# Kernel tuning notes

Hardware: AMD Instinct MI355X
Metric: run time of the kernel (lower is better)

The kernel has to match this reference:

```python
import jax, jax.numpy as jnp
import numpy as np

B, T, D = 4, 1024, 1024
H, DH = 8, 128           # heads, dim_head = dim // heads
E, FF = 8, 2048          # num_experts, expert hidden_dim
LN_EPS = 1e-5


def setup_inputs() -> dict:
    key = jax.random.key(0)
    ks = jax.random.split(key, 20)
    s = 0.02
    inp = {
        'v': jax.random.normal(ks[0], (B, T, D), jnp.float32),
        'k': jax.random.normal(ks[1], (B, T, D), jnp.float32),
        'q': jax.random.normal(ks[2], (B, T, D), jnp.float32),
        'noise': jax.random.normal(ks[3], (B * T, E), jnp.float32),
        # LayerNorm params (norm_v, norm_k, norm_q, norm_moe, moe output norm)
        'g_v': jnp.ones((D,)), 'b_v': jnp.zeros((D,)),
        'g_k': jnp.ones((D,)), 'b_k': jnp.zeros((D,)),
        'g_q': jnp.ones((D,)), 'b_q': jnp.zeros((D,)),
        'g_moe': jnp.ones((D,)), 'b_moe': jnp.zeros((D,)),
        'g_out': jnp.ones((D,)), 'b_out': jnp.zeros((D,)),
        # LinearAttention projections (q/k/v have no bias, out_proj has bias)
        'Wq': jax.random.normal(ks[4], (D, H * DH), jnp.float32) * s,
        'Wk': jax.random.normal(ks[5], (D, H * DH), jnp.float32) * s,
        'Wv': jax.random.normal(ks[6], (D, H * DH), jnp.float32) * s,
        'Wo': jax.random.normal(ks[7], (H * DH, D), jnp.float32) * s,
        'bo': jnp.zeros((D,)),
        # Router
        'Wr': jax.random.normal(ks[8], (D, E), jnp.float32) * s,
        'br': jnp.zeros((E,)),
        # Experts (stacked): dim -> FF -> dim
        'W1': jax.random.normal(ks[9], (E, D, FF), jnp.float32) * s,
        'b1': jnp.zeros((E, FF)),
        'W2': jax.random.normal(ks[10], (E, FF, D), jnp.float32) * s,
        'b2': jnp.zeros((E, D)),
        'top_k': 2,
    }
    return inp


def _ln(x, g, b):
    mu = x.mean(-1, keepdims=True)
    x0 = x - mu
    var = (x0 * x0).mean(-1, keepdims=True)
    return x0 * jax.lax.rsqrt(var + LN_EPS) * g + b


def reference(v, k, q, noise, g_v, b_v, g_k, b_k, g_q, b_q, g_moe, b_moe,
              g_out, b_out, Wq, Wk, Wv, Wo, bo, Wr, br, W1, b1, W2, b2, top_k):
    # --- LinearAttention over pre-normed v,k,q ---
    qh = jnp.einsum('btd,de->bte', _ln(q, g_q, b_q), Wq).reshape(B, T, H, DH)
    kh = jnp.einsum('btd,de->bte', _ln(k, g_k, b_k), Wk).reshape(B, T, H, DH)
    vh = jnp.einsum('btd,de->bte', _ln(v, g_v, b_v), Wv).reshape(B, T, H, DH)
    qf = jax.nn.elu(qh) + 1.0
    kf = jax.nn.elu(kh) + 1.0
    kv = jnp.einsum('bthd,bthe->bhde', kf, vh)          # [B,H,DH,DH]
    out = jnp.einsum('bthd,bhde->bthe', qf, kv)         # [B,T,H,DH]
    k_sum = kf.sum(axis=1) + 1e-6                       # [B,H,DH]
    denom = jnp.einsum('bthd,bhd->bth', qf, k_sum)[..., None]
    out = out / denom
    attn_out = jnp.einsum('bte,ed->btd', out.reshape(B, T, H * DH), Wo) + bo

    q_res = q + attn_out

    # --- MoEBlock: noisy top-k routing + expert MLPs + residual + LayerNorm ---
    x = _ln(q_res, g_moe, b_moe)
    xf = x.reshape(B * T, D)
    logits = xf @ Wr + br + noise * 0.1                 # noisy gating (randn/10)
    scores = jax.nn.softmax(logits, axis=-1)
    topk_s, topk_i = jax.lax.top_k(scores, top_k)       # [N,K]
    combine = (jax.nn.one_hot(topk_i, E, dtype=scores.dtype) * topk_s[..., None]).sum(1)  # [N,E]
    h = jax.nn.gelu(jnp.einsum('nd,edh->enh', xf, W1) + b1[:, None, :], approximate=False)
    eo = jnp.einsum('enh,ehd->end', h, W2) + b2[:, None, :]
    moe = jnp.einsum('end,ne->nd', eo, combine)         # weighted combine == masked dispatch
    moe_out = _ln(moe.reshape(B, T, D) + x, g_out, b_out)

    return q_res + moe_out
```

## Files before the change

kernel.cpp:

```cpp
#include <hip/hip_runtime.h>
#include <math.h>

typedef __attribute__((ext_vector_type(8))) short short8;
typedef __attribute__((ext_vector_type(4))) float f32x4;

#define LN_EPS 1e-5f

__device__ __forceinline__ float bf2f(unsigned short u) {
  unsigned int x = ((unsigned int)u) << 16;
  float f;
  __builtin_memcpy(&f, &x, 4);
  return f;
}
__device__ __forceinline__ unsigned short f2bf(float f) {
  unsigned int x;
  __builtin_memcpy(&x, &f, 4);
  x += 0x7fffu + ((x >> 16) & 1u);
  return (unsigned short)(x >> 16);
}

__device__ __forceinline__ void gload16(const void* g, void* l) {
  __builtin_amdgcn_global_load_lds(
      (__attribute__((address_space(1))) void*)(void*)g,
      (__attribute__((address_space(3))) void*)l, 16, 0, 0);
}

__device__ __forceinline__ void xcd_swizzle(int& bx, int& by) {
  const int nx = gridDim.x;
  const int nwg = nx * gridDim.y;
  const int orig = blockIdx.y * nx + blockIdx.x;
  const int cpx = nwg >> 3;
  const int lid = (orig & 7) * cpx + (orig >> 3);
  bx = lid % nx;
  by = lid / nx;
}

__device__ __forceinline__ void blockReduce2(float& a, float& b, float* s8) {
#pragma unroll
  for (int off = 32; off > 0; off >>= 1) {
    a += __shfl_down(a, off);
    b += __shfl_down(b, off);
  }
  const int w = threadIdx.x >> 6;
  if ((threadIdx.x & 63) == 0) { s8[w] = a; s8[4 + w] = b; }
  __syncthreads();
  a = s8[0] + s8[1] + s8[2] + s8[3];
  b = s8[4] + s8[5] + s8[6] + s8[7];
}

__global__ __launch_bounds__(256) void ln3_kernel(
    const float* __restrict__ q, const float* __restrict__ k, const float* __restrict__ v,
    const float* __restrict__ gq, const float* __restrict__ bq,
    const float* __restrict__ gk, const float* __restrict__ bk,
    const float* __restrict__ gv, const float* __restrict__ bv,
    unsigned short* __restrict__ oq, unsigned short* __restrict__ ok,
    unsigned short* __restrict__ ov) {
  __shared__ float s8[8];
  const int row = blockIdx.x, which = blockIdx.y;
  const float* x = which == 0 ? q : which == 1 ? k : v;
  const float* g = which == 0 ? gq : which == 1 ? gk : gv;
  const float* b = which == 0 ? bq : which == 1 ? bk : bv;
  unsigned short* o = which == 0 ? oq : which == 1 ? ok : ov;
  const float4 xv = ((const float4*)(x + (size_t)row * 1024))[threadIdx.x];
  float s = xv.x + xv.y + xv.z + xv.w;
  float s2 = xv.x * xv.x + xv.y * xv.y + xv.z * xv.z + xv.w * xv.w;
  blockReduce2(s, s2, s8);
  const float mu = s * (1.f / 1024.f);
  const float rs = rsqrtf(s2 * (1.f / 1024.f) - mu * mu + LN_EPS);
  const int c = threadIdx.x * 4;
  const float y[4] = {xv.x, xv.y, xv.z, xv.w};
#pragma unroll
  for (int j = 0; j < 4; ++j)
    o[(size_t)row * 1024 + c + j] = f2bf((y[j] - mu) * rs * g[c + j] + b[c + j]);
}

__global__ __launch_bounds__(256) void ln_moe_router_kernel(
    const float* __restrict__ qres, const float* __restrict__ g, const float* __restrict__ b,
    const float* __restrict__ Wr, const float* __restrict__ br,
    const float* __restrict__ noise,
    float* __restrict__ xf, unsigned short* __restrict__ xb,
    int* __restrict__ pick, float* __restrict__ pw) {
  __shared__ float s8[8];
  __shared__ float sacc[32];
  const int row = blockIdx.x;
  const float4 xv = ((const float4*)(qres + (size_t)row * 1024))[threadIdx.x];
  float s = xv.x + xv.y + xv.z + xv.w;
  float s2 = xv.x * xv.x + xv.y * xv.y + xv.z * xv.z + xv.w * xv.w;
  blockReduce2(s, s2, s8);
  const float mu = s * (1.f / 1024.f);
  const float rs = rsqrtf(s2 * (1.f / 1024.f) - mu * mu + LN_EPS);
  const int c = threadIdx.x * 4;
  const float yin[4] = {xv.x, xv.y, xv.z, xv.w};
  float y[4];
#pragma unroll
  for (int j = 0; j < 4; ++j) {
    y[j] = (yin[j] - mu) * rs * g[c + j] + b[c + j];
    xf[(size_t)row * 1024 + c + j] = y[j];
    xb[(size_t)row * 1024 + c + j] = f2bf(y[j]);
  }
  float acc[8] = {};
  const float4* wrv = (const float4*)(Wr + (size_t)c * 8);
#pragma unroll
  for (int j = 0; j < 4; ++j) {
    const float4 w0 = wrv[j * 2], w1 = wrv[j * 2 + 1];
    acc[0] += y[j] * w0.x; acc[1] += y[j] * w0.y;
    acc[2] += y[j] * w0.z; acc[3] += y[j] * w0.w;
    acc[4] += y[j] * w1.x; acc[5] += y[j] * w1.y;
    acc[6] += y[j] * w1.z; acc[7] += y[j] * w1.w;
  }
#pragma unroll
  for (int off = 32; off > 0; off >>= 1)
#pragma unroll
    for (int e = 0; e < 8; ++e) acc[e] += __shfl_down(acc[e], off);
  const int w = threadIdx.x >> 6;
  if ((threadIdx.x & 63) == 0)
#pragma unroll
    for (int e = 0; e < 8; ++e) sacc[w * 8 + e] = acc[e];
  __syncthreads();
  if (threadIdx.x == 0) {
    float lg[8], mx = -1e30f;
#pragma unroll
    for (int e = 0; e < 8; ++e) {
      lg[e] = sacc[e] + sacc[8 + e] + sacc[16 + e] + sacc[24 + e] + br[e] +
              0.1f * noise[(size_t)row * 8 + e];
      mx = fmaxf(mx, lg[e]);
    }
    float ssum = 0.f;
#pragma unroll
    for (int e = 0; e < 8; ++e) { lg[e] = expf(lg[e] - mx); ssum += lg[e]; }
    const float inv = 1.f / ssum;
#pragma unroll
    for (int e = 0; e < 8; ++e) lg[e] *= inv;
    int i1 = -1, i2 = -1;
    float m1 = -1.f, m2 = -1.f;
#pragma unroll
    for (int e = 0; e < 8; ++e) {
      if (lg[e] > m1) { m2 = m1; i2 = i1; m1 = lg[e]; i1 = e; }
      else if (lg[e] > m2) { m2 = lg[e]; i2 = e; }
    }
    pick[row * 2] = i1; pick[row * 2 + 1] = i2;
    pw[row * 2] = m1;  pw[row * 2 + 1] = m2;
  }
}

__global__ __launch_bounds__(1024) void route_build_kernel(
    const int* __restrict__ pick, const float* __restrict__ pw,
    int* __restrict__ seg, int* __restrict__ tok, float* __restrict__ wgt,
    int* __restrict__ slt) {
  __shared__ int cnt[8];
  __shared__ int segs[9];
  __shared__ int cur[8];
  const int tid = threadIdx.x;
  if (tid < 8) { cnt[tid] = 0; cur[tid] = 0; }
  __syncthreads();
  for (int i = tid; i < 8192; i += 1024) atomicAdd(&cnt[pick[i]], 1);
  __syncthreads();
  if (tid == 0) {
    int o = 0;
    for (int e = 0; e < 8; ++e) { segs[e] = o; o += (cnt[e] + 127) & ~127; }
    segs[8] = o;
  }
  __syncthreads();
  for (int i = tid; i < 9216; i += 1024) tok[i] = -1;
  if (tid < 9) seg[tid] = segs[tid];
  __syncthreads();
  for (int i = tid; i < 8192; i += 1024) {
    const int n = i >> 1, sl = i & 1;
    const int e = pick[i];
    const int p = atomicAdd(&cur[e], 1);
    const int gr = segs[e] + p;
    tok[gr] = n;
    wgt[gr] = pw[i];
    slt[gr] = sl;
  }
}

__global__ __launch_bounds__(256) void final_kernel(
    const float* __restrict__ eoS, const float* __restrict__ xf,
    const float* __restrict__ qres, const float* __restrict__ g,
    const float* __restrict__ b, float* __restrict__ out) {
  __shared__ float s8[8];
  const int row = blockIdx.x;
  const size_t SLOT = (size_t)4096 * 1024;
  const float4 m0 = ((const float4*)(eoS + (size_t)row * 1024))[threadIdx.x];
  const float4 m1 = ((const float4*)(eoS + SLOT + (size_t)row * 1024))[threadIdx.x];
  const float4 xv = ((const float4*)(xf + (size_t)row * 1024))[threadIdx.x];
  float y[4] = {m0.x + m1.x + xv.x, m0.y + m1.y + xv.y, m0.z + m1.z + xv.z,
                m0.w + m1.w + xv.w};
  float s = y[0] + y[1] + y[2] + y[3];
  float s2 = y[0] * y[0] + y[1] * y[1] + y[2] * y[2] + y[3] * y[3];
  blockReduce2(s, s2, s8);
  const float mu = s * (1.f / 1024.f);
  const float rs = rsqrtf(s2 * (1.f / 1024.f) - mu * mu + LN_EPS);
  const int c = threadIdx.x * 4;
#pragma unroll
  for (int j = 0; j < 4; ++j) {
    const size_t idx = (size_t)row * 1024 + c + j;
    out[idx] = qres[idx] + (y[j] - mu) * rs * g[c + j] + b[c + j];
  }
}

__global__ __launch_bounds__(256) void transposeB_kernel(
    const float* const* __restrict__ ins, unsigned short* const* __restrict__ outs,
    int R, int C) {
  __shared__ float t[32][33];
  const float* inz = ins[blockIdx.z];
  unsigned short* outz = outs[blockIdx.z];
  const int bx = blockIdx.x, by = blockIdx.y;
  const int tx = threadIdx.x & 31, ty = threadIdx.x >> 5;
#pragma unroll
  for (int i = 0; i < 32; i += 8)
    t[ty + i][tx] = inz[(size_t)(by * 32 + ty + i) * C + bx * 32 + tx];
  __syncthreads();
#pragma unroll
  for (int i = 0; i < 32; i += 8)
    outz[(size_t)(bx * 32 + ty + i) * R + by * 32 + tx] = f2bf(t[tx][ty + i]);
}

__global__ __launch_bounds__(256) void transpose8_kernel(
    const float* __restrict__ in, unsigned short* __restrict__ out, int R, int C) {
  __shared__ float t[32][33];
  const float* inz = in + (size_t)blockIdx.z * R * C;
  unsigned short* outz = out + (size_t)blockIdx.z * R * C;
  const int bx = blockIdx.x, by = blockIdx.y;
  const int tx = threadIdx.x & 31, ty = threadIdx.x >> 5;
#pragma unroll
  for (int i = 0; i < 32; i += 8)
    t[ty + i][tx] = inz[(size_t)(by * 32 + ty + i) * C + bx * 32 + tx];
  __syncthreads();
#pragma unroll
  for (int i = 0; i < 32; i += 8)
    outz[(size_t)(bx * 32 + ty + i) * R + by * 32 + tx] = f2bf(t[tx][ty + i]);
}

#define GEMM_STAGE(buf, k0, KD)                                              \
  gload16(gA0 + (k0), lA + (buf) * 4096);                                    \
  gload16(gA1 + (k0), lA + (buf) * 4096 + 16 * 32);                          \
  gload16(gB + (k0), lB + (buf) * 4096);                                     \
  gload16(gB + (size_t)16 * (KD) + (k0), lB + (buf) * 4096 + 16 * 32);

#define GEMM_COMPUTE(buf)                                                    \
  {                                                                          \
    const unsigned short* sA = &As[buf][0];                                  \
    const unsigned short* sB = &Bs[buf][0];                                  \
    short8 af[4], bfr[4];                                                    \
    _Pragma("unroll") for (int m = 0; m < 4; ++m)                            \
        af[m] = *(const short8*)&sA[(arow + m * 16) * 32 + kk];              \
    _Pragma("unroll") for (int n = 0; n < 4; ++n)                            \
        bfr[n] = *(const short8*)&sB[(brow + n * 16) * 32 + kk];             \
    _Pragma("unroll") for (int m = 0; m < 4; ++m)                            \
      _Pragma("unroll") for (int n = 0; n < 4; ++n)                          \
        acc[m][n] = __builtin_amdgcn_mfma_f32_16x16x32_bf16(                 \
            af[m], bfr[n], acc[m][n], 0, 0, 0);                              \
  }

#define GEMM_LOOP(KD)                                                        \
  GEMM_STAGE(0, 0, KD)                                                       \
  __syncthreads();                                                           \
  for (int k0 = 0; k0 < (KD); k0 += 64) {                                    \
    GEMM_STAGE(1, k0 + 32, KD)                                               \
    GEMM_COMPUTE(0)                                                          \
    __syncthreads();                                                         \
    if (k0 + 64 < (KD)) { GEMM_STAGE(0, k0 + 64, KD) }                       \
    GEMM_COMPUTE(1)                                                          \
    __syncthreads();                                                         \
  }

#define GEMM_PREAMBLE                                                        \
  __shared__ __align__(16) unsigned short As[2][128 * 32];                   \
  __shared__ __align__(16) unsigned short Bs[2][128 * 32];                   \
  const int tid = threadIdx.x;                                               \
  const int lane = tid & 63, w = tid >> 6;                                   \
  const int wr = w >> 1, wc = w & 1;                                         \
  const int sr = lane >> 2, sc = (lane & 3) * 8;                             \
  const int arow = wr * 64 + (lane & 15);                                    \
  const int brow = wc * 64 + (lane & 15);                                    \
  const int kk = (lane >> 4) * 8;                                            \
  unsigned short* lA = &As[0][(w * 32) * 32];                                \
  unsigned short* lB = &Bs[0][(w * 32) * 32];

__global__ __launch_bounds__(256) void gemm_qkv(
    const unsigned short* __restrict__ lnq, const unsigned short* __restrict__ lnk,
    const unsigned short* __restrict__ lnv, const unsigned short* __restrict__ WqT,
    const unsigned short* __restrict__ WkT, const unsigned short* __restrict__ WvT,
    unsigned short* __restrict__ qf, unsigned short* __restrict__ kf,
    unsigned short* __restrict__ vh) {
  const int z = blockIdx.z;
  const unsigned short* A = z == 0 ? lnq : z == 1 ? lnk : lnv;
  const unsigned short* Bt = z == 0 ? WqT : z == 1 ? WkT : WvT;
  unsigned short* outb = z == 0 ? qf : z == 1 ? kf : vh;
  const int K = 1024, N = 1024;
  GEMM_PREAMBLE
  int bx, by;
  xcd_swizzle(bx, by);
  const int row0 = by * 128, col0 = bx * 128;
  const unsigned short* gA0 = A + (size_t)(row0 + w * 32 + sr) * K + sc;
  const unsigned short* gA1 = gA0 + (size_t)16 * K;
  const unsigned short* gB = Bt + (size_t)(col0 + w * 32 + sr) * K + sc;
  f32x4 acc[4][4] = {};
  GEMM_LOOP(1024)
#pragma unroll
  for (int m = 0; m < 4; ++m) {
    const int rbase = row0 + wr * 64 + m * 16 + (lane >> 4) * 4;
#pragma unroll
    for (int n = 0; n < 4; ++n) {
      const int c = col0 + wc * 64 + n * 16 + (lane & 15);
#pragma unroll
      for (int r = 0; r < 4; ++r) {
        float v = acc[m][n][r];
        if (z < 2) v = v > 0.f ? v + 1.f : __expf(v);
        outb[(size_t)(rbase + r) * N + c] = f2bf(v);
      }
    }
  }
}

__global__ __launch_bounds__(256) void gemm_wo(
    const unsigned short* __restrict__ A, const unsigned short* __restrict__ Bt,
    float* __restrict__ outf, const float* __restrict__ bias,
    const float* __restrict__ addm) {
  const int K = 1024, N = 1024;
  GEMM_PREAMBLE
  int bx, by;
  xcd_swizzle(bx, by);
  const int row0 = by * 128, col0 = bx * 128;
  const unsigned short* gA0 = A + (size_t)(row0 + w * 32 + sr) * K + sc;
  const unsigned short* gA1 = gA0 + (size_t)16 * K;
  const unsigned short* gB = Bt + (size_t)(col0 + w * 32 + sr) * K + sc;
  f32x4 acc[4][4] = {};
  GEMM_LOOP(1024)
#pragma unroll
  for (int m = 0; m < 4; ++m) {
    const int rbase = row0 + wr * 64 + m * 16 + (lane >> 4) * 4;
#pragma unroll
    for (int n = 0; n < 4; ++n) {
      const int c = col0 + wc * 64 + n * 16 + (lane & 15);
#pragma unroll
      for (int r = 0; r < 4; ++r) {
        const size_t idx = (size_t)(rbase + r) * N + c;
        outf[idx] = acc[m][n][r] + bias[c] + addm[idx];
      }
    }
  }
}

template <int PHASE>
__global__ __launch_bounds__(256) void gemm_moe(
    const unsigned short* __restrict__ Asrc, const unsigned short* __restrict__ Ball,
    const float* __restrict__ bias_all, int Kdim, int N,
    const int* __restrict__ seg, const int* __restrict__ tok,
    const float* __restrict__ wgt, const int* __restrict__ slt,
    unsigned short* __restrict__ Hb, float* __restrict__ eoS) {
  const int K = PHASE == 1 ? 1024 : 2048;
  GEMM_PREAMBLE
  int bx, by;
  xcd_swizzle(bx, by);
  const int row0 = by * 128;
  if (row0 >= seg[8]) return;
  int e = 0;
  while (e < 7 && row0 >= seg[e + 1]) ++e;
  const int col0 = bx * 128;
  const unsigned short* Bt = Ball + (size_t)e * N * K;
  const int gr0 = row0 + w * 32 + sr;
  const int gr1 = gr0 + 16;
  const unsigned short* gA0;
  const unsigned short* gA1;
  if constexpr (PHASE == 1) {
    const int t0 = tok[gr0], t1 = tok[gr1];
    gA0 = Asrc + (size_t)(t0 < 0 ? 0 : t0) * K + sc;
    gA1 = Asrc + (size_t)(t1 < 0 ? 0 : t1) * K + sc;
  } else {
    gA0 = Asrc + (size_t)gr0 * K + sc;
    gA1 = Asrc + (size_t)gr1 * K + sc;
  }
  const unsigned short* gB = Bt + (size_t)(col0 + w * 32 + sr) * K + sc;
  f32x4 acc[4][4] = {};
  if constexpr (PHASE == 1) { GEMM_LOOP(1024) }
  else { GEMM_LOOP(2048) }
#pragma unroll
  for (int m = 0; m < 4; ++m) {
    const int rloc = wr * 64 + m * 16 + (lane >> 4) * 4;
#pragma unroll
    for (int n = 0; n < 4; ++n) {
      const int c = col0 + wc * 64 + n * 16 + (lane & 15);
#pragma unroll
      for (int r = 0; r < 4; ++r) {
        const int gr = row0 + rloc + r;
        float v = acc[m][n][r] + bias_all[(size_t)e * N + c];
        if constexpr (PHASE == 1) {
          v = 0.5f * v * (1.f + erff(v * 0.70710678118654752f));
          Hb[(size_t)gr * N + c] = f2bf(v);
        } else {
          const int t = tok[gr];
          if (t >= 0)
            eoS[(size_t)slt[gr] * (4096 * 1024) + (size_t)t * N + c] = wgt[gr] * v;
        }
      }
    }
  }
}

__global__ __launch_bounds__(256) void kvpart_kernel(
    const unsigned short* __restrict__ kf, const unsigned short* __restrict__ vh,
    float* __restrict__ kvp, float* __restrict__ ksp) {
  const int bh = blockIdx.x;
  const int b = bh >> 3, h = bh & 7;
  const int ch = blockIdx.y;
  const int tid = threadIdx.x;
  const int d0 = (tid >> 4) * 8, e0 = (tid & 15) * 8;
  __shared__ unsigned short kb[64][128];
  __shared__ unsigned short vb[64][128];
  for (int i = tid; i < 1024; i += 256) {
    const int tt = i >> 4, dd = (i & 15) * 8;
    const size_t base = ((size_t)((b * 1024 + ch * 64 + tt) * 8 + h)) * 128 + dd;
    *(short8*)&kb[tt][dd] = *(const short8*)&kf[base];
    *(short8*)&vb[tt][dd] = *(const short8*)&vh[base];
  }
  __syncthreads();
  float acc[8][8] = {};
  float ks[8] = {};
  for (int tt = 0; tt < 64; ++tt) {
    float kv8[8], vv8[8];
    const short8 kr = *(const short8*)&kb[tt][d0];
    const short8 vr = *(const short8*)&vb[tt][e0];
#pragma unroll
    for (int j = 0; j < 8; ++j) {
      kv8[j] = bf2f((unsigned short)kr[j]);
      vv8[j] = bf2f((unsigned short)vr[j]);
    }
#pragma unroll
    for (int i = 0; i < 8; ++i)
#pragma unroll
      for (int j = 0; j < 8; ++j) acc[i][j] += kv8[i] * vv8[j];
    if ((tid & 15) == 0)
#pragma unroll
      for (int i = 0; i < 8; ++i) ks[i] += kv8[i];
  }
  const size_t obase = ((size_t)(ch * 32 + bh) * 128) * 128;
#pragma unroll
  for (int i = 0; i < 8; ++i)
#pragma unroll
    for (int j = 0; j < 8; ++j)
      kvp[obase + (size_t)(d0 + i) * 128 + e0 + j] = acc[i][j];
  if ((tid & 15) == 0)
#pragma unroll
    for (int i = 0; i < 8; ++i) ksp[(size_t)(ch * 32 + bh) * 128 + d0 + i] = ks[i];
}

__global__ __launch_bounds__(256) void kvreduce_kernel(
    const float* __restrict__ kvp, const float* __restrict__ ksp,
    unsigned short* __restrict__ kvb, float* __restrict__ ksum) {
  const int idx = blockIdx.x * 256 + threadIdx.x;
  const int CS = 32 * 128 * 128;
  float s = 0.f;
#pragma unroll
  for (int c = 0; c < 16; ++c) s += kvp[(size_t)c * CS + idx];
  kvb[idx] = f2bf(s);
  if (idx < 32 * 128) {
    float t = 1e-6f;
#pragma unroll
    for (int c = 0; c < 16; ++c) t += ksp[c * 4096 + idx];
    ksum[idx] = t;
  }
}

__global__ __launch_bounds__(256) void attnout_kernel(
    const unsigned short* __restrict__ qf, const unsigned short* __restrict__ kvb,
    const float* __restrict__ ksum, unsigned short* __restrict__ ctx) {
  const int bh = blockIdx.x, b = bh >> 3, h = bh & 7;
  const int tb = blockIdx.y;
  const int tid = threadIdx.x;
  __shared__ unsigned short kvl[128 * 128];
  __shared__ float ksl[128];
  __shared__ float denom[128];
  __shared__ unsigned short qfl[128 * 32];
  for (int i = tid; i < 16384; i += 256) kvl[i] = kvb[(size_t)bh * 16384 + i];
  if (tid < 128) ksl[tid] = ksum[bh * 128 + tid];
  __syncthreads();
  if (tid < 128) {
    const int t = tb * 128 + tid;
    const size_t qbase = ((size_t)((b * 1024 + t) * 8 + h)) * 128;
    float s = 0.f;
    for (int d = 0; d < 128; ++d) s += bf2f(qf[qbase + d]) * ksl[d];
    denom[tid] = s;
  }
  float acc[8][8] = {};
  const int t0 = (tid >> 4) * 8, e0 = (tid & 15) * 8;
  for (int dc = 0; dc < 128; dc += 32) {
    __syncthreads();
    for (int i = tid; i < 128 * 32; i += 256) {
      const int tt = i >> 5, dd = i & 31;
      qfl[i] = qf[((size_t)((b * 1024 + tb * 128 + tt) * 8 + h)) * 128 + dc + dd];
    }
    __syncthreads();
    for (int dd = 0; dd < 32; ++dd) {
      float kvrow[8];
#pragma unroll
      for (int j = 0; j < 8; ++j) kvrow[j] = bf2f(kvl[(dc + dd) * 128 + e0 + j]);
#pragma unroll
      for (int i = 0; i < 8; ++i) {
        const float qv = bf2f(qfl[(t0 + i) * 32 + dd]);
#pragma unroll
        for (int j = 0; j < 8; ++j) acc[i][j] += qv * kvrow[j];
      }
    }
  }
  __syncthreads();
#pragma unroll
  for (int i = 0; i < 8; ++i) {
    const int t = tb * 128 + t0 + i;
    const float inv = 1.f / denom[t0 + i];
#pragma unroll
    for (int j = 0; j < 8; ++j)
      ctx[((size_t)(b * 1024 + t)) * 1024 + h * 128 + e0 + j] = f2bf(acc[i][j] * inv);
  }
}

__global__ void setptr_kernel(const float* Wq, const float* Wk, const float* Wv,
                              const float* Wo, unsigned short* WqT, unsigned short* WkT,
                              unsigned short* WvT, unsigned short* WoT,
                              const float** ins, unsigned short** outs) {
  if (threadIdx.x == 0) {
    ins[0] = Wq; ins[1] = Wk; ins[2] = Wv; ins[3] = Wo;
    outs[0] = WqT; outs[1] = WkT; outs[2] = WvT; outs[3] = WoT;
  }
}

extern "C" void kernel_launch(void* const* d_in, const int* in_sizes, int n_in,
                              void* d_out, int out_size, void* d_ws, size_t ws_size,
                              hipStream_t stream) {
  (void)in_sizes; (void)n_in; (void)out_size; (void)ws_size;
  const float* vin  = (const float*)d_in[0];
  const float* kin  = (const float*)d_in[1];
  const float* qin  = (const float*)d_in[2];
  const float* noise = (const float*)d_in[3];
  const float* g_v = (const float*)d_in[4];  const float* b_v = (const float*)d_in[5];
  const float* g_k = (const float*)d_in[6];  const float* b_k = (const float*)d_in[7];
  const float* g_q = (const float*)d_in[8];  const float* b_q = (const float*)d_in[9];
  const float* g_moe = (const float*)d_in[10]; const float* b_moe = (const float*)d_in[11];
  const float* g_out = (const float*)d_in[12]; const float* b_out = (const float*)d_in[13];
  const float* Wq = (const float*)d_in[14];
  const float* Wk = (const float*)d_in[15];
  const float* Wv = (const float*)d_in[16];
  const float* Wo = (const float*)d_in[17];
  const float* bo = (const float*)d_in[18];
  const float* Wr = (const float*)d_in[19];
  const float* br = (const float*)d_in[20];
  const float* W1 = (const float*)d_in[21];
  const float* b1 = (const float*)d_in[22];
  const float* W2 = (const float*)d_in[23];
  const float* b2 = (const float*)d_in[24];
  float* out = (float*)d_out;

  const int NT = 4096, D = 1024, FF = 2048;
  const int MAXR = 9216;

  char* p = (char*)d_ws;
  auto alloc = [&](size_t bytes) {
    void* r = (void*)p;
    p += (bytes + 255) & ~(size_t)255;
    return r;
  };
  char* base0 = p;
  unsigned short* lnq = (unsigned short*)alloc((size_t)NT * D * 2);
  unsigned short* lnk = (unsigned short*)alloc((size_t)NT * D * 2);
  unsigned short* lnv = (unsigned short*)alloc((size_t)NT * D * 2);
  unsigned short* WqT = (unsigned short*)alloc((size_t)D * D * 2);
  unsigned short* WkT = (unsigned short*)alloc((size_t)D * D * 2);
  unsigned short* WvT = (unsigned short*)alloc((size_t)D * D * 2);
  unsigned short* WoT = (unsigned short*)alloc((size_t)D * D * 2);
  unsigned short* qf  = (unsigned short*)alloc((size_t)NT * D * 2);
  unsigned short* kf  = (unsigned short*)alloc((size_t)NT * D * 2);
  unsigned short* vh  = (unsigned short*)alloc((size_t)NT * D * 2);
  unsigned short* kvb = (unsigned short*)alloc((size_t)32 * 128 * 128 * 2);
  float* ksp  = (float*)alloc((size_t)16 * 32 * 128 * 4);
  float* ksum = (float*)alloc((size_t)32 * 128 * 4);
  unsigned short* ctx = (unsigned short*)alloc((size_t)NT * D * 2);
  float* qres = (float*)alloc((size_t)NT * D * 4);
  float* xf   = (float*)alloc((size_t)NT * D * 4);
  unsigned short* xb = (unsigned short*)alloc((size_t)NT * D * 2);
  unsigned short* W1T_all = (unsigned short*)alloc((size_t)8 * D * FF * 2);
  unsigned short* W2T_all = (unsigned short*)alloc((size_t)8 * FF * D * 2);
  float* eoS = (float*)alloc((size_t)2 * NT * D * 4);
  int* pick = (int*)alloc((size_t)NT * 2 * 4);
  float* pw = (float*)alloc((size_t)NT * 2 * 4);
  int* seg = (int*)alloc(9 * 4);
  int* tokl = (int*)alloc(MAXR * 4);
  float* wgt = (float*)alloc(MAXR * 4);
  int* slt = (int*)alloc(MAXR * 4);
  const float** tins = (const float**)alloc(4 * sizeof(void*));
  unsigned short** touts = (unsigned short**)alloc(4 * sizeof(void*));
  float* kvp = eoS;
  unsigned short* Hb = (unsigned short*)base0;

  setptr_kernel<<<dim3(1), 64, 0, stream>>>(Wq, Wk, Wv, Wo, WqT, WkT, WvT, WoT,
                                            tins, touts);
  transposeB_kernel<<<dim3(32, 32, 4), 256, 0, stream>>>(tins, touts, D, D);

  ln3_kernel<<<dim3(NT, 3), 256, 0, stream>>>(qin, kin, vin, g_q, b_q, g_k, b_k, g_v, b_v,
                                              lnq, lnk, lnv);

  gemm_qkv<<<dim3(D / 128, NT / 128, 3), 256, 0, stream>>>(lnq, lnk, lnv, WqT, WkT, WvT,
                                                           qf, kf, vh);

  kvpart_kernel<<<dim3(32, 16), 256, 0, stream>>>(kf, vh, kvp, ksp);
  kvreduce_kernel<<<dim3(2048), 256, 0, stream>>>(kvp, ksp, kvb, ksum);
  attnout_kernel<<<dim3(32, 8), 256, 0, stream>>>(qf, kvb, ksum, ctx);

  gemm_wo<<<dim3(D / 128, NT / 128), 256, 0, stream>>>(ctx, WoT, qres, bo, qin);

  ln_moe_router_kernel<<<dim3(NT), 256, 0, stream>>>(qres, g_moe, b_moe, Wr, br, noise,
                                                     xf, xb, pick, pw);
  route_build_kernel<<<dim3(1), 1024, 0, stream>>>(pick, pw, seg, tokl, wgt, slt);

  transpose8_kernel<<<dim3(FF / 32, D / 32, 8), 256, 0, stream>>>(W1, W1T_all, D, FF);
  transpose8_kernel<<<dim3(D / 32, FF / 32, 8), 256, 0, stream>>>(W2, W2T_all, FF, D);

  gemm_moe<1><<<dim3(FF / 128, MAXR / 128), 256, 0, stream>>>(
      xb, W1T_all, b1, 1024, FF, seg, tokl, wgt, slt, Hb, nullptr);
  gemm_moe<2><<<dim3(D / 128, MAXR / 128), 256, 0, stream>>>(
      Hb, W2T_all, b2, 2048, D, seg, tokl, wgt, slt, nullptr, eoS);

  final_kernel<<<dim3(NT), 256, 0, stream>>>(eoS, xf, qres, g_out, b_out, out);
}
```

Measured before the change: 388.8 us.

## Rewrite MoE expert GEMMs as 8-wave 256-row tiles with staged LDS pipeline

Replaces the 128x128, 4-wave MoE grouped GEMM with an 8-wave, 512-thread kernel. It uses 256-row tiles (256 columns for the first expert GEMM, 128 for the second), XOR-swizzled double-buffered LDS, direct global-to-LDS loads interleaved with four MFMA quadrants per k-step, and raised wave priority around the MFMAs. Expert segments are now padded to 256 rows, so the routing buffers and grid grow to 10240 rows. The aim is more data reuse per tile and overlap of loads with compute. The cost is more padded wasted rows, more register pressure with two blocks per CU, and fewer blocks in the grid.

After: 492.9 us. +26.8%, slower.

```diff
diff --git a/kernel.cpp b/kernel.cpp
--- a/kernel.cpp
+++ b/kernel.cpp
@@ -157,11 +157,11 @@
   __syncthreads();
   if (tid == 0) {
     int o = 0;
-    for (int e = 0; e < 8; ++e) { segs[e] = o; o += (cnt[e] + 127) & ~127; }
+    for (int e = 0; e < 8; ++e) { segs[e] = o; o += (cnt[e] + 255) & ~255; }
     segs[8] = o;
   }
   __syncthreads();
-  for (int i = tid; i < 9216; i += 1024) tok[i] = -1;
+  for (int i = tid; i < 10240; i += 1024) tok[i] = -1;
   if (tid < 9) seg[tid] = segs[tid];
   __syncthreads();
   for (int i = tid; i < 8192; i += 1024) {
@@ -344,60 +344,162 @@
   }
 }
 
+#define MOE_ISSUE_A(buf, k0, p)                                               \
+  gload16((const char*)pA[p] + (size_t)(k0) * 2 + cbs,                        \
+          (char*)&As[buf][0] + (p) * 8192 + wid * 1024);
+#define MOE_ISSUE_B(buf, k0, p)                                               \
+  gload16((const char*)pB[p] + (size_t)(k0) * 2 + cbs,                        \
+          (char*)&Bs[buf][0] + (p) * 8192 + wid * 1024);
+
+#define MOE_LDA(buf, qm, adst)                                                \
+  _Pragma("unroll") for (int mf = 0; mf < 4; ++mf)                            \
+  _Pragma("unroll") for (int ks = 0; ks < 2; ++ks) {                          \
+    const int rrow = wr * 128 + (qm) * 64 + mf * 16 + (lane & 15);            \
+    const int bofs =                                                          \
+        (rrow * 128 + ks * 64 + (lane >> 4) * 16) ^ ((lane & 7) << 4);        \
+    adst[mf][ks] = *(const short8*)((const char*)&As[buf][0] + bofs);         \
+  }
+#define MOE_LDB(buf, qn, bdst)                                                \
+  _Pragma("unroll") for (int nf = 0; nf < NF2; ++nf)                          \
+  _Pragma("unroll") for (int ks = 0; ks < 2; ++ks) {                          \
+    const int rrow = wcol * (BN / 4) + (qn) * (BN / 8) + nf * 16 + (lane & 15); \
+    const int bofs =                                                          \
+        (rrow * 128 + ks * 64 + (lane >> 4) * 16) ^ ((lane & 7) << 4);        \
+    bdst[nf][ks] = *(const short8*)((const char*)&Bs[buf][0] + bofs);         \
+  }
+#define MOE_MFMA(qm, qn, areg, breg)                                          \
+  __builtin_amdgcn_s_setprio(1);                                              \
+  _Pragma("unroll") for (int mf = 0; mf < 4; ++mf)                            \
+  _Pragma("unroll") for (int nf = 0; nf < NF2; ++nf)                          \
+  _Pragma("unroll") for (int ks = 0; ks < 2; ++ks)                            \
+    acc[qm][qn][mf][nf] = __builtin_amdgcn_mfma_f32_16x16x32_bf16(            \
+        areg[mf][ks], breg[nf][ks], acc[qm][qn][mf][nf], 0, 0, 0);            \
+  __builtin_amdgcn_s_setprio(0);
+#define MOE_LGKM0 asm volatile("s_waitcnt lgkmcnt(0)" ::: "memory");
+#define MOE_BAR __builtin_amdgcn_s_barrier();
+
 template <int PHASE>
-__global__ __launch_bounds__(256) void gemm_moe(
+__global__ __launch_bounds__(512, 2) void gemm_moe8(
     const unsigned short* __restrict__ Asrc, const unsigned short* __restrict__ Ball,
-    const float* __restrict__ bias_all, int Kdim, int N,
+    const float* __restrict__ bias_all,
     const int* __restrict__ seg, const int* __restrict__ tok,
     const float* __restrict__ wgt, const int* __restrict__ slt,
     unsigned short* __restrict__ Hb, float* __restrict__ eoS) {
-  const int K = PHASE == 1 ? 1024 : 2048;
-  GEMM_PREAMBLE
+  constexpr int K = (PHASE == 1) ? 1024 : 2048;
+  constexpr int N = (PHASE == 1) ? 2048 : 1024;
+  constexpr int BN = (PHASE == 1) ? 256 : 128;
+  constexpr int NF2 = BN / 128;
+  constexpr int NB = BN / 64;
+  constexpr int KT = K / 64;
+  __shared__ __align__(16) unsigned short As[2][256 * 64];
+  __shared__ __align__(16) unsigned short Bs[2][BN * 64];
+  const int tid = threadIdx.x;
+  const int lane = tid & 63, wid = tid >> 6;
+  const int wr = wid >> 2, wcol = wid & 3;
   int bx, by;
-  xcd_swizzle(bx, by);
-  const int row0 = by * 128;
+  {
+    const int nx = gridDim.x, nwg = nx * gridDim.y;
+    const int orig = blockIdx.y * nx + blockIdx.x;
+    const int cpx = nwg >> 3;
+    const int lid = (orig & 7) * cpx + (orig >> 3);
+    bx = lid % nx;
+    by = lid / nx;
+  }
+  const int row0 = by * 256;
   if (row0 >= seg[8]) return;
   int e = 0;
   while (e < 7 && row0 >= seg[e + 1]) ++e;
-  const int col0 = bx * 128;
+  const int col0 = bx * BN;
   const unsigned short* Bt = Ball + (size_t)e * N * K;
-  const int gr0 = row0 + w * 32 + sr;
-  const int gr1 = gr0 + 16;
-  const unsigned short* gA0;
-  const unsigned short* gA1;
-  if constexpr (PHASE == 1) {
-    const int t0 = tok[gr0], t1 = tok[gr1];
-    gA0 = Asrc + (size_t)(t0 < 0 ? 0 : t0) * K + sc;
-    gA1 = Asrc + (size_t)(t1 < 0 ? 0 : t1) * K + sc;
-  } else {
-    gA0 = Asrc + (size_t)gr0 * K + sc;
-    gA1 = Asrc + (size_t)gr1 * K + sc;
-  }
-  const unsigned short* gB = Bt + (size_t)(col0 + w * 32 + sr) * K + sc;
-  f32x4 acc[4][4] = {};
-  if constexpr (PHASE == 1) { GEMM_LOOP(1024) }
-  else { GEMM_LOOP(2048) }
-#pragma unroll
-  for (int m = 0; m < 4; ++m) {
-    const int rloc = wr * 64 + m * 16 + (lane >> 4) * 4;
-#pragma unroll
-    for (int n = 0; n < 4; ++n) {
-      const int c = col0 + wc * 64 + n * 16 + (lane & 15);
-#pragma unroll
-      for (int r = 0; r < 4; ++r) {
-        const int gr = row0 + rloc + r;
-        float v = acc[m][n][r] + bias_all[(size_t)e * N + c];
-        if constexpr (PHASE == 1) {
-          v = 0.5f * v * (1.f + erff(v * 0.70710678118654752f));
-          Hb[(size_t)gr * N + c] = f2bf(v);
-        } else {
-          const int t = tok[gr];
-          if (t >= 0)
-            eoS[(size_t)slt[gr] * (4096 * 1024) + (size_t)t * N + c] = wgt[gr] * v;
+
+  const int srow = tid >> 3;
+  const int cbs = ((tid & 7) * 16) ^ ((srow & 7) << 4);
+  const unsigned short* pA[4];
+  const unsigned short* pB[NB];
+#pragma unroll
+  for (int p = 0; p < 4; ++p) {
+    const int gr = row0 + p * 64 + srow;
+    int rowid;
+    if constexpr (PHASE == 1) {
+      const int t0 = tok[gr];
+      rowid = t0 < 0 ? 0 : t0;
+    } else {
+      rowid = gr;
+    }
+    pA[p] = Asrc + (size_t)rowid * K;
+  }
+#pragma unroll
+  for (int p = 0; p < NB; ++p)
+    pB[p] = Bt + (size_t)(col0 + p * 64 + srow) * K;
+
+  f32x4 acc[2][2][4][NF2] = {};
+  short8 a[4][2], b0[NF2][2], b1[NF2][2];
+
+  MOE_ISSUE_A(0, 0, 0) MOE_ISSUE_A(0, 0, 1) MOE_ISSUE_A(0, 0, 2) MOE_ISSUE_A(0, 0, 3)
+  MOE_ISSUE_B(0, 0, 0)
+  if constexpr (NB > 1) { MOE_ISSUE_B(0, 0, 1) }
+  if constexpr (NB > 2) { MOE_ISSUE_B(0, 0, 2) MOE_ISSUE_B(0, 0, 3) }
+  asm volatile("s_waitcnt vmcnt(0)" ::: "memory");
+  MOE_BAR
+
+  for (int t = 0; t < KT; ++t) {
+    const int cur = t & 1, nxt = cur ^ 1;
+    const int k1 = (t + 1) * 64;
+    const bool more = (t + 1 < KT);
+    if (more) { MOE_ISSUE_A(nxt, k1, 0) MOE_ISSUE_A(nxt, k1, 1) MOE_ISSUE_B(nxt, k1, 0) }
+    MOE_LDA(cur, 0, a)
+    MOE_LDB(cur, 0, b0)
+    MOE_MFMA(0, 0, a, b0)
+    MOE_LGKM0
+    MOE_BAR
+    if (more) {
+      MOE_ISSUE_A(nxt, k1, 2) MOE_ISSUE_A(nxt, k1, 3)
+      if constexpr (NB > 1) { MOE_ISSUE_B(nxt, k1, 1) }
+      if constexpr (NB > 2) { MOE_ISSUE_B(nxt, k1, 2) }
+    }
+    MOE_LDB(cur, 1, b1)
+    MOE_MFMA(0, 1, a, b1)
+    MOE_LGKM0
+    MOE_BAR
+    if (more) {
+      if constexpr (NB > 2) { MOE_ISSUE_B(nxt, k1, 3) }
+    }
+    MOE_LDA(cur, 1, a)
+    MOE_MFMA(1, 1, a, b1)
+    MOE_LGKM0
+    MOE_BAR
+    MOE_MFMA(1, 0, a, b0)
+    if (more) asm volatile("s_waitcnt vmcnt(0)" ::: "memory");
+    MOE_BAR
+  }
+
+  const float* bias = bias_all + (size_t)e * N;
+#pragma unroll
+  for (int qm = 0; qm < 2; ++qm)
+#pragma unroll
+    for (int mf = 0; mf < 4; ++mf) {
+      const int rloc = wr * 128 + qm * 64 + mf * 16 + (lane >> 4) * 4;
+#pragma unroll
+      for (int qn = 0; qn < 2; ++qn)
+#pragma unroll
+        for (int nf = 0; nf < NF2; ++nf) {
+          const int c = col0 + wcol * (BN / 4) + qn * (BN / 8) + nf * 16 + (lane & 15);
+#pragma unroll
+          for (int r = 0; r < 4; ++r) {
+            const int gr = row0 + rloc + r;
+            float v = acc[qm][qn][mf][nf][r] + bias[c];
+            if constexpr (PHASE == 1) {
+              v = 0.5f * v * (1.f + erff(v * 0.70710678118654752f));
+              Hb[(size_t)gr * 2048 + c] = f2bf(v);
+            } else {
+              const int tkn = tok[gr];
+              if (tkn >= 0)
+                eoS[(size_t)slt[gr] * (4096 * 1024) + (size_t)tkn * 1024 + c] =
+                    wgt[gr] * v;
+            }
+          }
         }
-      }
-    }
-  }
+    }
 }
 
 __global__ __launch_bounds__(256) void kvpart_kernel(
@@ -553,7 +655,7 @@
   float* out = (float*)d_out;
 
   const int NT = 4096, D = 1024, FF = 2048;
-  const int MAXR = 9216;
+  const int MAXR = 10240;
 
   char* p = (char*)d_ws;
   auto alloc = [&](size_t bytes) {
@@ -616,10 +718,10 @@
   transpose8_kernel<<<dim3(FF / 32, D / 32, 8), 256, 0, stream>>>(W1, W1T_all, D, FF);
   transpose8_kernel<<<dim3(D / 32, FF / 32, 8), 256, 0, stream>>>(W2, W2T_all, FF, D);
 
-  gemm_moe<1><<<dim3(FF / 128, MAXR / 128), 256, 0, stream>>>(
-      xb, W1T_all, b1, 1024, FF, seg, tokl, wgt, slt, Hb, nullptr);
-  gemm_moe<2><<<dim3(D / 128, MAXR / 128), 256, 0, stream>>>(
-      Hb, W2T_all, b2, 2048, D, seg, tokl, wgt, slt, nullptr, eoS);
+  gemm_moe8<1><<<dim3(FF / 256, MAXR / 256), 512, 0, stream>>>(
+      xb, W1T_all, b1, seg, tokl, wgt, slt, Hb, nullptr);
+  gemm_moe8<2><<<dim3(D / 128, MAXR / 256), 512, 0, stream>>>(
+      Hb, W2T_all, b2, seg, tokl, wgt, slt, nullptr, eoS);
 
   final_kernel<<<dim3(NT), 256, 0, stream>>>(eoS, xf, qres, g_out, b_out, out);
 }
```

## Rework bf16 GEMM core with K=64 tiles, XOR-swizzled LDS and vmcnt pipelining

Applied to the files above, without the earlier changes.

Replaces the shared GEMM macros with a new core that stages 128x64 K-tiles per buffer instead of 128x32. LDS addresses get an XOR swizzle so fragment reads avoid bank conflicts. Loads for tile t+2 are issued while tile t is computed, using explicit s_waitcnt vmcnt and raw barriers instead of __syncthreads, and s_setprio is raised around the MFMA block. LDS use doubles to 64KB per block, which may lower occupancy. The fine-grained waitcnt logic is fragile if the load count per stage changes.

New measurement: 411.9 us. 6.0% more time.

```diff
diff --git a/kernel.cpp b/kernel.cpp
--- a/kernel.cpp
+++ b/kernel.cpp
@@ -233,51 +233,67 @@
     outz[(size_t)(bx * 32 + ty + i) * R + by * 32 + tx] = f2bf(t[tx][ty + i]);
 }
 
-#define GEMM_STAGE(buf, k0, KD)                                              \
-  gload16(gA0 + (k0), lA + (buf) * 4096);                                    \
-  gload16(gA1 + (k0), lA + (buf) * 4096 + 16 * 32);                          \
-  gload16(gB + (k0), lB + (buf) * 4096);                                     \
-  gload16(gB + (size_t)16 * (KD) + (k0), lB + (buf) * 4096 + 16 * 32);
-
-#define GEMM_COMPUTE(buf)                                                    \
-  {                                                                          \
-    const unsigned short* sA = &As[buf][0];                                  \
-    const unsigned short* sB = &Bs[buf][0];                                  \
-    short8 af[4], bfr[4];                                                    \
-    _Pragma("unroll") for (int m = 0; m < 4; ++m)                            \
-        af[m] = *(const short8*)&sA[(arow + m * 16) * 32 + kk];              \
-    _Pragma("unroll") for (int n = 0; n < 4; ++n)                            \
-        bfr[n] = *(const short8*)&sB[(brow + n * 16) * 32 + kk];             \
-    _Pragma("unroll") for (int m = 0; m < 4; ++m)                            \
-      _Pragma("unroll") for (int n = 0; n < 4; ++n)                          \
-        acc[m][n] = __builtin_amdgcn_mfma_f32_16x16x32_bf16(                 \
-            af[m], bfr[n], acc[m][n], 0, 0, 0);                              \
-  }
-
-#define GEMM_LOOP(KD)                                                        \
-  GEMM_STAGE(0, 0, KD)                                                       \
-  __syncthreads();                                                           \
-  for (int k0 = 0; k0 < (KD); k0 += 64) {                                    \
-    GEMM_STAGE(1, k0 + 32, KD)                                               \
-    GEMM_COMPUTE(0)                                                          \
-    __syncthreads();                                                         \
-    if (k0 + 64 < (KD)) { GEMM_STAGE(0, k0 + 64, KD) }                       \
-    GEMM_COMPUTE(1)                                                          \
-    __syncthreads();                                                         \
-  }
-
-#define GEMM_PREAMBLE                                                        \
-  __shared__ __align__(16) unsigned short As[2][128 * 32];                   \
-  __shared__ __align__(16) unsigned short Bs[2][128 * 32];                   \
-  const int tid = threadIdx.x;                                               \
-  const int lane = tid & 63, w = tid >> 6;                                   \
-  const int wr = w >> 1, wc = w & 1;                                         \
-  const int sr = lane >> 2, sc = (lane & 3) * 8;                             \
-  const int arow = wr * 64 + (lane & 15);                                    \
-  const int brow = wc * 64 + (lane & 15);                                    \
-  const int kk = (lane >> 4) * 8;                                            \
-  unsigned short* lA = &As[0][(w * 32) * 32];                                \
-  unsigned short* lB = &Bs[0][(w * 32) * 32];
+#define CORE_PREAMBLE                                                         \
+  __shared__ __align__(16) unsigned short As[2][128 * 64];                    \
+  __shared__ __align__(16) unsigned short Bs[2][128 * 64];                    \
+  const int tid = threadIdx.x;                                                \
+  const int lane = tid & 63, wid = tid >> 6;                                  \
+  const int wr = wid >> 1, wc = wid & 1;                                      \
+  const int cbs = ((tid & 7) * 16) ^ (((tid >> 3) & 7) << 4);
+
+#define CORE_STAGE(buf, kt)                                                   \
+  _Pragma("unroll") for (int p = 0; p < 4; ++p)                               \
+      gload16((const char*)pA[p] + (size_t)(kt) * 128 + cbs,                  \
+              (char*)&As[buf][0] + p * 4096 + wid * 1024);                    \
+  _Pragma("unroll") for (int p = 0; p < 4; ++p)                               \
+      gload16((const char*)pB[p] + (size_t)(kt) * 128 + cbs,                  \
+              (char*)&Bs[buf][0] + p * 4096 + wid * 1024);
+
+#define CORE_COMPUTE(buf)                                                     \
+  {                                                                           \
+    short8 a[4][2], b[4][2];                                                  \
+    _Pragma("unroll") for (int mf = 0; mf < 4; ++mf)                          \
+    _Pragma("unroll") for (int ks = 0; ks < 2; ++ks) {                        \
+      const int rr = wr * 64 + mf * 16 + (lane & 15);                         \
+      const int bofs =                                                        \
+          (rr * 128 + ks * 64 + (lane >> 4) * 16) ^ ((rr & 7) << 4);          \
+      a[mf][ks] = *(const short8*)((const char*)&As[buf][0] + bofs);          \
+    }                                                                         \
+    _Pragma("unroll") for (int nf = 0; nf < 4; ++nf)                          \
+    _Pragma("unroll") for (int ks = 0; ks < 2; ++ks) {                        \
+      const int rr = wc * 64 + nf * 16 + (lane & 15);                         \
+      const int bofs =                                                        \
+          (rr * 128 + ks * 64 + (lane >> 4) * 16) ^ ((rr & 7) << 4);          \
+      b[nf][ks] = *(const short8*)((const char*)&Bs[buf][0] + bofs);          \
+    }                                                                         \
+    __builtin_amdgcn_s_setprio(1);                                            \
+    _Pragma("unroll") for (int mf = 0; mf < 4; ++mf)                          \
+    _Pragma("unroll") for (int nf = 0; nf < 4; ++nf)                          \
+    _Pragma("unroll") for (int ks = 0; ks < 2; ++ks)                          \
+        acc[mf][nf] = __builtin_amdgcn_mfma_f32_16x16x32_bf16(                \
+            a[mf][ks], b[nf][ks], acc[mf][nf], 0, 0, 0);                      \
+    __builtin_amdgcn_s_setprio(0);                                            \
+  }
+
+#define CORE_LOOP(KT)                                                         \
+  CORE_STAGE(0, 0)                                                            \
+  CORE_STAGE(1, 1)                                                            \
+  asm volatile("s_waitcnt vmcnt(8)" ::: "memory");                            \
+  __builtin_amdgcn_s_barrier();                                               \
+  for (int t = 0; t < (KT); ++t) {                                            \
+    const int cur = t & 1;                                                    \
+    CORE_COMPUTE(cur)                                                         \
+    if (t + 1 < (KT)) {                                                       \
+      __builtin_amdgcn_s_barrier();                                           \
+      if (t + 2 < (KT)) {                                                     \
+        CORE_STAGE(cur, t + 2)                                                \
+        asm volatile("s_waitcnt vmcnt(8)" ::: "memory");                      \
+      } else {                                                                \
+        asm volatile("s_waitcnt vmcnt(0)" ::: "memory");                      \
+      }                                                                       \
+      __builtin_amdgcn_s_barrier();                                           \
+    }                                                                         \
+  }
 
 __global__ __launch_bounds__(256) void gemm_qkv(
     const unsigned short* __restrict__ lnq, const unsigned short* __restrict__ lnk,
@@ -290,15 +306,19 @@
   const unsigned short* Bt = z == 0 ? WqT : z == 1 ? WkT : WvT;
   unsigned short* outb = z == 0 ? qf : z == 1 ? kf : vh;
   const int K = 1024, N = 1024;
-  GEMM_PREAMBLE
+  CORE_PREAMBLE
   int bx, by;
   xcd_swizzle(bx, by);
   const int row0 = by * 128, col0 = bx * 128;
-  const unsigned short* gA0 = A + (size_t)(row0 + w * 32 + sr) * K + sc;
-  const unsigned short* gA1 = gA0 + (size_t)16 * K;
-  const unsigned short* gB = Bt + (size_t)(col0 + w * 32 + sr) * K + sc;
+  const unsigned short* pA[4];
+  const unsigned short* pB[4];
+#pragma unroll
+  for (int p = 0; p < 4; ++p) {
+    pA[p] = A + (size_t)(row0 + p * 32 + (tid >> 3)) * K;
+    pB[p] = Bt + (size_t)(col0 + p * 32 + (tid >> 3)) * K;
+  }
   f32x4 acc[4][4] = {};
-  GEMM_LOOP(1024)
+  CORE_LOOP(16)
 #pragma unroll
   for (int m = 0; m < 4; ++m) {
     const int rbase = row0 + wr * 64 + m * 16 + (lane >> 4) * 4;
@@ -320,15 +340,19 @@
     float* __restrict__ outf, const float* __restrict__ bias,
     const float* __restrict__ addm) {
   const int K = 1024, N = 1024;
-  GEMM_PREAMBLE
+  CORE_PREAMBLE
   int bx, by;
   xcd_swizzle(bx, by);
   const int row0 = by * 128, col0 = bx * 128;
-  const unsigned short* gA0 = A + (size_t)(row0 + w * 32 + sr) * K + sc;
-  const unsigned short* gA1 = gA0 + (size_t)16 * K;
-  const unsigned short* gB = Bt + (size_t)(col0 + w * 32 + sr) * K + sc;
+  const unsigned short* pA[4];
+  const unsigned short* pB[4];
+#pragma unroll
+  for (int p = 0; p < 4; ++p) {
+    pA[p] = A + (size_t)(row0 + p * 32 + (tid >> 3)) * K;
+    pB[p] = Bt + (size_t)(col0 + p * 32 + (tid >> 3)) * K;
+  }
   f32x4 acc[4][4] = {};
-  GEMM_LOOP(1024)
+  CORE_LOOP(16)
 #pragma unroll
   for (int m = 0; m < 4; ++m) {
     const int rbase = row0 + wr * 64 + m * 16 + (lane >> 4) * 4;
@@ -347,12 +371,14 @@
 template <int PHASE>
 __global__ __launch_bounds__(256) void gemm_moe(
     const unsigned short* __restrict__ Asrc, const unsigned short* __restrict__ Ball,
-    const float* __restrict__ bias_all, int Kdim, int N,
+    const float* __restrict__ bias_all,
     const int* __restrict__ seg, const int* __restrict__ tok,
     const float* __restrict__ wgt, const int* __restrict__ slt,
     unsigned short* __restrict__ Hb, float* __restrict__ eoS) {
-  const int K = PHASE == 1 ? 1024 : 2048;
-  GEMM_PREAMBLE
+  constexpr int K = (PHASE == 1) ? 1024 : 2048;
+  constexpr int N = (PHASE == 1) ? 2048 : 1024;
+  constexpr int KT = K / 64;
+  CORE_PREAMBLE
   int bx, by;
   xcd_swizzle(bx, by);
   const int row0 = by * 128;
@@ -361,22 +387,24 @@
   while (e < 7 && row0 >= seg[e + 1]) ++e;
   const int col0 = bx * 128;
   const unsigned short* Bt = Ball + (size_t)e * N * K;
-  const int gr0 = row0 + w * 32 + sr;
-  const int gr1 = gr0 + 16;
-  const unsigned short* gA0;
-  const unsigned short* gA1;
-  if constexpr (PHASE == 1) {
-    const int t0 = tok[gr0], t1 = tok[gr1];
-    gA0 = Asrc + (size_t)(t0 < 0 ? 0 : t0) * K + sc;
-    gA1 = Asrc + (size_t)(t1 < 0 ? 0 : t1) * K + sc;
-  } else {
-    gA0 = Asrc + (size_t)gr0 * K + sc;
-    gA1 = Asrc + (size_t)gr1 * K + sc;
-  }
-  const unsigned short* gB = Bt + (size_t)(col0 + w * 32 + sr) * K + sc;
+  const unsigned short* pA[4];
+  const unsigned short* pB[4];
+#pragma unroll
+  for (int p = 0; p < 4; ++p) {
+    const int gr = row0 + p * 32 + (tid >> 3);
+    int rowid;
+    if constexpr (PHASE == 1) {
+      const int t0 = tok[gr];
+      rowid = t0 < 0 ? 0 : t0;
+    } else {
+      rowid = gr;
+    }
+    pA[p] = Asrc + (size_t)rowid * K;
+    pB[p] = Bt + (size_t)(col0 + p * 32 + (tid >> 3)) * K;
+  }
   f32x4 acc[4][4] = {};
-  if constexpr (PHASE == 1) { GEMM_LOOP(1024) }
-  else { GEMM_LOOP(2048) }
+  CORE_LOOP(KT)
+  const float* bias = bias_all + (size_t)e * N;
 #pragma unroll
   for (int m = 0; m < 4; ++m) {
     const int rloc = wr * 64 + m * 16 + (lane >> 4) * 4;
@@ -386,14 +414,15 @@
 #pragma unroll
       for (int r = 0; r < 4; ++r) {
         const int gr = row0 + rloc + r;
-        float v = acc[m][n][r] + bias_all[(size_t)e * N + c];
+        float v = acc[m][n][r] + bias[c];
         if constexpr (PHASE == 1) {
           v = 0.5f * v * (1.f + erff(v * 0.70710678118654752f));
-          Hb[(size_t)gr * N + c] = f2bf(v);
+          Hb[(size_t)gr * 2048 + c] = f2bf(v);
         } else {
-          const int t = tok[gr];
-          if (t >= 0)
-            eoS[(size_t)slt[gr] * (4096 * 1024) + (size_t)t * N + c] = wgt[gr] * v;
+          const int tkn = tok[gr];
+          if (tkn >= 0)
+            eoS[(size_t)slt[gr] * (4096 * 1024) + (size_t)tkn * 1024 + c] =
+                wgt[gr] * v;
         }
       }
     }
@@ -617,9 +646,9 @@
   transpose8_kernel<<<dim3(D / 32, FF / 32, 8), 256, 0, stream>>>(W2, W2T_all, FF, D);
 
   gemm_moe<1><<<dim3(FF / 128, MAXR / 128), 256, 0, stream>>>(
-      xb, W1T_all, b1, 1024, FF, seg, tokl, wgt, slt, Hb, nullptr);
+      xb, W1T_all, b1, seg, tokl, wgt, slt, Hb, nullptr);
   gemm_moe<2><<<dim3(D / 128, MAXR / 128), 256, 0, stream>>>(
-      Hb, W2T_all, b2, 2048, D, seg, tokl, wgt, slt, nullptr, eoS);
+      Hb, W2T_all, b2, seg, tokl, wgt, slt, nullptr, eoS);
 
   final_kernel<<<dim3(NT), 256, 0, stream>>>(eoS, xf, qres, g_out, b_out, out);
 }
```
